# Kernel tuning notes

Hardware: AMD Instinct MI355X
Metric: run time of the kernel (lower is better)

## Reference

```python
import jax, jax.numpy as jnp
import numpy as np
from jax import lax

NUM_HEADS = 8
EPS = 1e-12  # torch F.normalize eps


def setup_inputs() -> dict:
    key = jax.random.key(0)
    ks = jax.random.split(key, 5)
    dim = 192
    b, h, w = 8, 128, 128
    return {
        "x": jax.random.normal(ks[0], (b, dim, h, w), jnp.float32),
        "w_qkv": jax.random.normal(ks[1], (3 * dim, dim, 1, 1), jnp.float32) * (1.0 / np.sqrt(dim)),
        "w_dw": jax.random.normal(ks[2], (3 * dim, 1, 3, 3), jnp.float32) * (1.0 / 3.0),
        "w_proj": jax.random.normal(ks[3], (dim, dim, 1, 1), jnp.float32) * (1.0 / np.sqrt(dim)),
        "temperature": jnp.ones((NUM_HEADS, 1, 1), jnp.float32),
    }


def _l2norm(t):
    n = jnp.sqrt(jnp.sum(t * t, axis=-1, keepdims=True))
    return t / jnp.maximum(n, EPS)


def reference(x, w_qkv, w_dw, w_proj, temperature):
    b, c, h, w = x.shape
    # 1x1 conv to 3*dim channels
    qkv = jnp.einsum('bchw,oc->bohw', x, w_qkv[:, :, 0, 0])
    # depthwise 3x3 conv, dilation=2, padding=2, groups=3*dim
    qkv = lax.conv_general_dilated(
        qkv, w_dw, window_strides=(1, 1), padding=((2, 2), (2, 2)),
        rhs_dilation=(2, 2), feature_group_count=3 * c,
        dimension_numbers=('NCHW', 'OIHW', 'NCHW'))
    q, k, v = jnp.split(qkv, 3, axis=1)
    ch = c // NUM_HEADS
    def heads(t):  # b (head ch) h w -> b head ch (h w)
        return t.reshape(b, NUM_HEADS, ch, h * w)
    q, k, v = heads(q), heads(k), heads(v)
    q = _l2norm(q)
    k = _l2norm(k)
    attn = jnp.einsum('bhcn,bhdn->bhcd', q, k) * temperature  # (b, head, ch, ch)
    attn = jax.nn.softmax(attn, axis=-1)
    out = jnp.einsum('bhcd,bhdn->bhcn', attn, v)
    out = out.reshape(b, c, h, w)
    out = jnp.einsum('bchw,oc->bohw', out, w_proj[:, :, 0, 0])
    return out
```

## Files before the change

### kernel.cpp

```cpp
#include <hip/hip_runtime.h>


#define DIM 192
#define NH 8
#define CH 24
#define IH 128
#define IW 128
#define NPIX (IH*IW)
#define BATCH 8
#define QKVC (3*DIM)
#define PAD 200
#define SPAD 264

typedef unsigned short u16;
typedef short bf16x8 __attribute__((ext_vector_type(8)));
typedef float f32x4 __attribute__((ext_vector_type(4)));

__device__ __forceinline__ float b2f(u16 u){
    unsigned v = ((unsigned)u) << 16;
    return __builtin_bit_cast(float, v);
}
__device__ __forceinline__ u16 f2b(float f){
    unsigned u = __builtin_bit_cast(unsigned, f);
    u += 0x7fffu + ((u >> 16) & 1u);
    return (u16)(u >> 16);
}

__device__ __forceinline__ void conv_row8(const u16* __restrict__ rp, int px0,
        float w0, float w1, float w2, float* o_){
    float f[12];
    if(px0 > 0){
        unsigned u = *(const unsigned*)(rp + px0 - 2);
        f[0] = b2f((u16)u); f[1] = b2f((u16)(u >> 16));
    } else { f[0] = 0.f; f[1] = 0.f; }
    bf16x8 v = *(const bf16x8*)(rp + px0);
    #pragma unroll
    for(int j=0;j<8;j++) f[2+j] = b2f((u16)v[j]);
    if(px0 < 120){
        unsigned u = *(const unsigned*)(rp + px0 + 8);
        f[10] = b2f((u16)u); f[11] = b2f((u16)(u >> 16));
    } else { f[10] = 0.f; f[11] = 0.f; }
    #pragma unroll
    for(int i=0;i<8;i++) o_[i] += w0*f[i] + w1*f[i+2] + w2*f[i+4];
}

__global__ __launch_bounds__(256) void k0_wcvt(const float* __restrict__ wqkv,
        u16* __restrict__ wb){
    int i = (blockIdx.x*256 + threadIdx.x)*4;
    f32x4 v = *(const f32x4*)&wqkv[i];
    unsigned lo = ((unsigned)f2b(v[1]) << 16) | f2b(v[0]);
    unsigned hi = ((unsigned)f2b(v[3]) << 16) | f2b(v[2]);
    *(uint2*)&wb[i] = make_uint2(lo, hi);
}

__global__ __launch_bounds__(256) void k1_qkv(const float* __restrict__ x,
        const u16* __restrict__ wb, u16* __restrict__ qkv_pre){
    __shared__ __align__(16) u16 Xl[128*PAD];
    const int tid = threadIdx.x;
    const int pt = blockIdx.x, b = blockIdx.y;
    const int p0 = pt*128;
    {
        const int px = tid & 127, half = tid >> 7;
        const float* xb = x + (size_t)b*DIM*NPIX + p0 + px;
        for(int cg = 0; cg < 12; cg++){
            int cb = half*96 + cg*8;
            bf16x8 v;
            #pragma unroll
            for(int j=0;j<8;j++) v[j] = (short)f2b(xb[(size_t)(cb+j)*NPIX]);
            *(bf16x8*)&Xl[px*PAD + cb] = v;
        }
    }
    __syncthreads();
    const int lane = tid & 63, w = tid >> 6;
    const int r = lane & 15, quad = lane >> 4;
    const int mbase = (w & 1)*32, nbase = (w >> 1)*64;
    u16* op = qkv_pre + (size_t)b*QKVC*NPIX + p0;
    for(int ot = 0; ot < 9; ot++){
        const int obase = ot*64;
        f32x4 acc[8];
        { f32x4 z = {0.f,0.f,0.f,0.f}; for(int i=0;i<8;i++) acc[i]=z; }
        const u16* w0p = wb + (size_t)(obase + mbase + r)*DIM;
        const u16* w1p = w0p + 16*DIM;
        #pragma unroll
        for(int kk = 0; kk < 6; kk++){
            const int k0 = kk*32 + quad*8;
            bf16x8 a0 = *(const bf16x8*)&w0p[k0];
            bf16x8 a1 = *(const bf16x8*)&w1p[k0];
            #pragma unroll
            for(int ni=0; ni<4; ni++){
                bf16x8 bb = *(const bf16x8*)&Xl[(nbase + ni*16 + r)*PAD + k0];
                acc[ni*2+0] = __builtin_amdgcn_mfma_f32_16x16x32_bf16(bb, a0, acc[ni*2+0], 0,0,0);
                acc[ni*2+1] = __builtin_amdgcn_mfma_f32_16x16x32_bf16(bb, a1, acc[ni*2+1], 0,0,0);
            }
        }
        #pragma unroll
        for(int ni=0; ni<4; ni++)
            #pragma unroll
            for(int mi=0; mi<2; mi++){
                int o = obase + mbase + mi*16 + r;
                int px = nbase + ni*16 + quad*4;
                f32x4 a = acc[ni*2+mi];
                unsigned lo = ((unsigned)f2b(a[1]) << 16) | f2b(a[0]);
                unsigned hi = ((unsigned)f2b(a[3]) << 16) | f2b(a[2]);
                *(uint2*)&op[(size_t)o*NPIX + px] = make_uint2(lo, hi);
            }
    }
}

__global__ __launch_bounds__(256) void k2_gram(const u16* __restrict__ qkv_pre,
        const float* __restrict__ wdw, float* __restrict__ G){
    __shared__ __align__(16) u16 Sl[48*SPAD];
    const int tid = threadIdx.x;
    const int pc = blockIdx.x, h = blockIdx.y, b = blockIdx.z;
    const int lane = tid & 63, w = tid >> 6;
    const int r = lane & 15, quad = lane >> 4;
    f32x4 acc[6];
    { f32x4 z = {0.f,0.f,0.f,0.f}; for(int i=0;i<6;i++) acc[i]=z; }
    for(int chunk = 0; chunk < 2; chunk++){
        if(chunk) __syncthreads();
        for(int it = 0; it < 6; it++){
            int t = tid + it*256;
            int c48 = t >> 5, oct = t & 31;
            int isK = (c48 >= CH);
            int c = isK ? (c48 - CH) : c48;
            int ch = (isK ? DIM : 0) + h*CH + c;
            const u16* base = qkv_pre + ((size_t)b*QKVC + ch)*NPIX;
            const float* wv = wdw + ch*9;
            int py = pc*4 + chunk*2 + (oct >> 4);
            int px0 = (oct & 15)*8;
            float o_[8];
            #pragma unroll
            for(int i=0;i<8;i++) o_[i]=0.f;
            #pragma unroll
            for(int ky=0;ky<3;ky++){
                int ry = py + 2*ky - 2;
                if(ry < 0 || ry >= IH) continue;
                conv_row8(base + ry*IW, px0, wv[ky*3], wv[ky*3+1], wv[ky*3+2], o_);
            }
            bf16x8 v;
            #pragma unroll
            for(int i=0;i<8;i++) v[i] = (short)f2b(o_[i]);
            *(bf16x8*)&Sl[c48*SPAD + oct*8] = v;
        }
        __syncthreads();
        #pragma unroll
        for(int kk = 0; kk < 2; kk++){
            const int k0 = w*64 + kk*32 + quad*8;
            bf16x8 f0 = *(const bf16x8*)&Sl[(     r)*SPAD + k0];
            bf16x8 f1 = *(const bf16x8*)&Sl[(16 + r)*SPAD + k0];
            bf16x8 f2 = *(const bf16x8*)&Sl[(32 + r)*SPAD + k0];
            acc[0] = __builtin_amdgcn_mfma_f32_16x16x32_bf16(f0, f0, acc[0], 0,0,0);
            acc[1] = __builtin_amdgcn_mfma_f32_16x16x32_bf16(f0, f1, acc[1], 0,0,0);
            acc[2] = __builtin_amdgcn_mfma_f32_16x16x32_bf16(f0, f2, acc[2], 0,0,0);
            acc[3] = __builtin_amdgcn_mfma_f32_16x16x32_bf16(f1, f1, acc[3], 0,0,0);
            acc[4] = __builtin_amdgcn_mfma_f32_16x16x32_bf16(f1, f2, acc[4], 0,0,0);
            acc[5] = __builtin_amdgcn_mfma_f32_16x16x32_bf16(f2, f2, acc[5], 0,0,0);
        }
    }
    __syncthreads();
    float* R = (float*)Sl;
    #pragma unroll
    for(int tile=0; tile<6; tile++)
        *(f32x4*)&R[(w*6 + tile)*256 + lane*4] = acc[tile];
    __syncthreads();
    float* Gb = G + (size_t)(b*NH + h)*48*48;
    #pragma unroll
    for(int i=0; i<6; i++){
        int idx = tid + i*256;
        int tile = idx >> 8, rem = idx & 255;
        int ln = rem >> 2, t = rem & 3;
        float s = R[idx] + R[1536 + idx] + R[2*1536 + idx] + R[3*1536 + idx];
        int ti = (tile<3) ? 0 : ((tile<5) ? 1 : 2);
        int tj = (tile<3) ? tile : ((tile<5) ? (tile-2) : 2);
        int c = ti*16 + (ln >> 4)*4 + t;
        int d = tj*16 + (ln & 15);
        atomicAdd(&Gb[c*48 + d], s);
    }
}

__global__ __launch_bounds__(256) void k4_vconv(u16* __restrict__ qkv_pre,
        const float* __restrict__ wdw){
    const int tid = threadIdx.x;
    const int oct = tid & 15, pyl = tid >> 4;
    const int band = blockIdx.x, cp = blockIdx.y, b = blockIdx.z;
    const int py = band*16 + pyl, px0 = oct*8;
    #pragma unroll
    for(int j=0;j<2;j++){
        int ch = cp*2 + j;
        const u16* base = qkv_pre + ((size_t)b*QKVC + 2*DIM + ch)*NPIX;
        const float* wv = wdw + (2*DIM + ch)*9;
        float o_[8];
        #pragma unroll
        for(int i=0;i<8;i++) o_[i]=0.f;
        #pragma unroll
        for(int ky=0;ky<3;ky++){
            int ry = py + 2*ky - 2;
            if(ry < 0 || ry >= IH) continue;
            conv_row8(base + ry*IW, px0, wv[ky*3], wv[ky*3+1], wv[ky*3+2], o_);
        }
        bf16x8 v;
        #pragma unroll
        for(int i=0;i<8;i++) v[i] = (short)f2b(o_[i]);
        *(bf16x8*)&qkv_pre[((size_t)b*QKVC + ch)*NPIX + py*IW + px0] = v;
    }
}

__global__ __launch_bounds__(256) void k3_attn(const float* __restrict__ G,
        const float* __restrict__ temp, const float* __restrict__ wproj,
        u16* __restrict__ M){
    __shared__ float attn[NH][CH][CH];
    __shared__ float nq[DIM], nk[DIM];
    const int b = blockIdx.x, tid = threadIdx.x;
    const float* Gb = G + (size_t)b*NH*48*48;
    if(tid < DIM){
        int h = tid / CH, c = tid % CH;
        const float* g = Gb + (size_t)h*48*48;
        nq[tid] = fmaxf(sqrtf(g[c*48 + c]), 1e-12f);
        nk[tid] = fmaxf(sqrtf(g[(CH+c)*48 + (CH+c)]), 1e-12f);
    }
    __syncthreads();
    if(tid < DIM){
        int h = tid / CH, c = tid % CH;
        float t = temp[h];
        const float* g = Gb + (size_t)h*48*48 + c*48 + CH;
        float row[CH];
        float mx = -1e30f;
        #pragma unroll
        for(int d=0; d<CH; d++){
            float v = g[d] / (nq[tid]*nk[h*CH+d]) * t;
            row[d]=v; mx = fmaxf(mx,v);
        }
        float sum=0.f;
        #pragma unroll
        for(int d=0;d<CH;d++){ row[d]=expf(row[d]-mx); sum+=row[d]; }
        float inv = 1.f/sum;
        #pragma unroll
        for(int d=0;d<CH;d++) attn[h][c][d] = row[d]*inv;
    }
    __syncthreads();
    u16* Mb = M + (size_t)b*DIM*DIM;
    for(int i = tid; i < DIM*DIM; i += 256){
        int o = i / DIM, hd = i % DIM;
        int h = hd / CH, d = hd % CH;
        float s = 0.f;
        #pragma unroll
        for(int c=0;c<CH;c++)
            s += wproj[o*DIM + h*CH + c] * attn[h][c][d];
        Mb[i] = f2b(s);
    }
}

__global__ __launch_bounds__(256) void k5_out(const u16* __restrict__ qkv_pre,
        const u16* __restrict__ M, float* __restrict__ out){
    __shared__ __align__(16) u16 vl[128*PAD];
    const int tid = threadIdx.x;
    const int py = blockIdx.x, b = blockIdx.y;
    const int p0 = py*IW;
    {
        const int px = tid & 127, half = tid >> 7;
        const u16* vb = qkv_pre + (size_t)b*QKVC*NPIX + p0 + px;
        for(int cg = 0; cg < 12; cg++){
            int cb = half*96 + cg*8;
            bf16x8 v;
            #pragma unroll
            for(int j=0;j<8;j++) v[j] = (short)vb[(size_t)(cb+j)*NPIX];
            *(bf16x8*)&vl[px*PAD + cb] = v;
        }
    }
    __syncthreads();
    const int lane = tid & 63, w = tid >> 6;
    const int r = lane & 15, quad = lane >> 4;
    const int mbase = (w & 1)*32, nbase = (w >> 1)*64;
    const u16* Mb = M + (size_t)b*DIM*DIM;
    for(int ot = 0; ot < 3; ot++){
        const int obase = ot*64;
        f32x4 acc[8];
        { f32x4 z = {0.f,0.f,0.f,0.f}; for(int i=0;i<8;i++) acc[i]=z; }
        const u16* m0 = Mb + (size_t)(obase + mbase + r)*DIM;
        const u16* m1 = m0 + 16*DIM;
        #pragma unroll
        for(int kk = 0; kk < 6; kk++){
            const int k0 = kk*32 + quad*8;
            bf16x8 a0 = *(const bf16x8*)&m0[k0];
            bf16x8 a1 = *(const bf16x8*)&m1[k0];
            #pragma unroll
            for(int ni=0; ni<4; ni++){
                bf16x8 bb = *(const bf16x8*)&vl[(nbase + ni*16 + r)*PAD + k0];
                acc[ni*2+0] = __builtin_amdgcn_mfma_f32_16x16x32_bf16(a0, bb, acc[ni*2+0], 0,0,0);
                acc[ni*2+1] = __builtin_amdgcn_mfma_f32_16x16x32_bf16(a1, bb, acc[ni*2+1], 0,0,0);
            }
        }
        float* op = out + ((size_t)b*DIM + obase)*NPIX + p0;
        #pragma unroll
        for(int ni=0; ni<4; ni++)
            #pragma unroll
            for(int mi=0; mi<2; mi++){
                int o_loc = mbase + mi*16 + quad*4;
                int p_loc = nbase + ni*16 + r;
                #pragma unroll
                for(int t=0;t<4;t++)
                    op[(size_t)(o_loc+t)*NPIX + p_loc] = acc[ni*2+mi][t];
            }
    }
}

extern "C" void kernel_launch(void* const* d_in, const int* in_sizes, int n_in,
                              void* d_out, int out_size, void* d_ws, size_t ws_size,
                              hipStream_t stream){
    const float* x     = (const float*)d_in[0];
    const float* wqkv  = (const float*)d_in[1];
    const float* wdw   = (const float*)d_in[2];
    const float* wproj = (const float*)d_in[3];
    const float* temp  = (const float*)d_in[4];
    float* out = (float*)d_out;

    char* ws = (char*)d_ws;
    u16* qkv_pre = (u16*)ws;
    size_t off = (size_t)BATCH*QKVC*NPIX*sizeof(u16);
    float* G  = (float*)(ws + off); off += (size_t)BATCH*NH*48*48*4;
    u16* M    = (u16*)(ws + off);   off += (size_t)BATCH*DIM*DIM*2;
    u16* wb   = (u16*)(ws + off);   off += (size_t)QKVC*DIM*2;

    hipMemsetAsync(G, 0, (size_t)BATCH*NH*48*48*sizeof(float), stream);

    k0_wcvt<<<108, 256, 0, stream>>>(wqkv, wb);
    k1_qkv <<<dim3(128, BATCH), 256, 0, stream>>>(x, wb, qkv_pre);
    k2_gram<<<dim3(32, NH, BATCH), 256, 0, stream>>>(qkv_pre, wdw, G);
    k4_vconv<<<dim3(8, 96, BATCH), 256, 0, stream>>>(qkv_pre, wdw);
    k3_attn<<<BATCH, 256, 0, stream>>>(G, temp, wproj, M);
    k5_out <<<dim3(128, BATCH), 256, 0, stream>>>(qkv_pre, M, out);
}
```

Baseline: 433.8 us.

## Halve pixel tiles in QKV and output GEMMs, split output channels per wave

Both the QKV projection and the output projection kernels now process 64 pixels per block instead of 128. That doubles the grid and halves LDS use per block, which should raise occupancy on the many-CU GPU. Each wave now owns a disjoint set of 16-row output-channel tiles across all 64 pixels, rather than a 32x64 quadrant. The output kernel swaps MFMA operand order so each lane writes contiguous pixels with a 16-byte vector store instead of scalar strided stores. In exchange, each weight fragment is reused across fewer pixels and each block re-reads the weights more often.

New measurement: 435.0 us. No clear change (+0.3%).

```diff
diff --git a/kernel.cpp b/kernel.cpp
--- a/kernel.cpp
+++ b/kernel.cpp
@@ -55,15 +55,16 @@
 
 __global__ __launch_bounds__(256) void k1_qkv(const float* __restrict__ x,
         const u16* __restrict__ wb, u16* __restrict__ qkv_pre){
-    __shared__ __align__(16) u16 Xl[128*PAD];
+    __shared__ __align__(16) u16 Xl[64*PAD];
     const int tid = threadIdx.x;
     const int pt = blockIdx.x, b = blockIdx.y;
-    const int p0 = pt*128;
+    const int p0 = pt*64;
     {
-        const int px = tid & 127, half = tid >> 7;
+        const int px = tid & 63, grp = tid >> 6;
         const float* xb = x + (size_t)b*DIM*NPIX + p0 + px;
-        for(int cg = 0; cg < 12; cg++){
-            int cb = half*96 + cg*8;
+        #pragma unroll
+        for(int cg = 0; cg < 6; cg++){
+            int cb = grp*48 + cg*8;
             bf16x8 v;
             #pragma unroll
             for(int j=0;j<8;j++) v[j] = (short)f2b(xb[(size_t)(cb+j)*NPIX]);
@@ -73,37 +74,31 @@
     __syncthreads();
     const int lane = tid & 63, w = tid >> 6;
     const int r = lane & 15, quad = lane >> 4;
-    const int mbase = (w & 1)*32, nbase = (w >> 1)*64;
     u16* op = qkv_pre + (size_t)b*QKVC*NPIX + p0;
-    for(int ot = 0; ot < 9; ot++){
-        const int obase = ot*64;
-        f32x4 acc[8];
-        { f32x4 z = {0.f,0.f,0.f,0.f}; for(int i=0;i<8;i++) acc[i]=z; }
-        const u16* w0p = wb + (size_t)(obase + mbase + r)*DIM;
-        const u16* w1p = w0p + 16*DIM;
+    for(int i = 0; i < 9; i++){
+        const int ob = (w*9 + i)*16;
+        f32x4 acc[4];
+        { f32x4 z = {0.f,0.f,0.f,0.f}; for(int j=0;j<4;j++) acc[j]=z; }
+        const u16* wp = wb + (size_t)(ob + r)*DIM;
         #pragma unroll
         for(int kk = 0; kk < 6; kk++){
             const int k0 = kk*32 + quad*8;
-            bf16x8 a0 = *(const bf16x8*)&w0p[k0];
-            bf16x8 a1 = *(const bf16x8*)&w1p[k0];
+            bf16x8 a0 = *(const bf16x8*)&wp[k0];
             #pragma unroll
             for(int ni=0; ni<4; ni++){
-                bf16x8 bb = *(const bf16x8*)&Xl[(nbase + ni*16 + r)*PAD + k0];
-                acc[ni*2+0] = __builtin_amdgcn_mfma_f32_16x16x32_bf16(bb, a0, acc[ni*2+0], 0,0,0);
-                acc[ni*2+1] = __builtin_amdgcn_mfma_f32_16x16x32_bf16(bb, a1, acc[ni*2+1], 0,0,0);
+                bf16x8 bb = *(const bf16x8*)&Xl[(ni*16 + r)*PAD + k0];
+                acc[ni] = __builtin_amdgcn_mfma_f32_16x16x32_bf16(bb, a0, acc[ni], 0,0,0);
             }
         }
         #pragma unroll
-        for(int ni=0; ni<4; ni++)
-            #pragma unroll
-            for(int mi=0; mi<2; mi++){
-                int o = obase + mbase + mi*16 + r;
-                int px = nbase + ni*16 + quad*4;
-                f32x4 a = acc[ni*2+mi];
-                unsigned lo = ((unsigned)f2b(a[1]) << 16) | f2b(a[0]);
-                unsigned hi = ((unsigned)f2b(a[3]) << 16) | f2b(a[2]);
-                *(uint2*)&op[(size_t)o*NPIX + px] = make_uint2(lo, hi);
-            }
+        for(int ni=0; ni<4; ni++){
+            int o = ob + r;
+            int px = ni*16 + quad*4;
+            f32x4 a = acc[ni];
+            unsigned lo = ((unsigned)f2b(a[1]) << 16) | f2b(a[0]);
+            unsigned hi = ((unsigned)f2b(a[3]) << 16) | f2b(a[2]);
+            *(uint2*)&op[(size_t)o*NPIX + px] = make_uint2(lo, hi);
+        }
     }
 }
 
@@ -252,15 +247,16 @@
 
 __global__ __launch_bounds__(256) void k5_out(const u16* __restrict__ qkv_pre,
         const u16* __restrict__ M, float* __restrict__ out){
-    __shared__ __align__(16) u16 vl[128*PAD];
+    __shared__ __align__(16) u16 vl[64*PAD];
     const int tid = threadIdx.x;
-    const int py = blockIdx.x, b = blockIdx.y;
-    const int p0 = py*IW;
+    const int pt = blockIdx.x, b = blockIdx.y;
+    const int p0 = pt*64;
     {
-        const int px = tid & 127, half = tid >> 7;
+        const int px = tid & 63, grp = tid >> 6;
         const u16* vb = qkv_pre + (size_t)b*QKVC*NPIX + p0 + px;
-        for(int cg = 0; cg < 12; cg++){
-            int cb = half*96 + cg*8;
+        #pragma unroll
+        for(int cg = 0; cg < 6; cg++){
+            int cb = grp*48 + cg*8;
             bf16x8 v;
             #pragma unroll
             for(int j=0;j<8;j++) v[j] = (short)vb[(size_t)(cb+j)*NPIX];
@@ -270,37 +266,26 @@
     __syncthreads();
     const int lane = tid & 63, w = tid >> 6;
     const int r = lane & 15, quad = lane >> 4;
-    const int mbase = (w & 1)*32, nbase = (w >> 1)*64;
     const u16* Mb = M + (size_t)b*DIM*DIM;
-    for(int ot = 0; ot < 3; ot++){
-        const int obase = ot*64;
-        f32x4 acc[8];
-        { f32x4 z = {0.f,0.f,0.f,0.f}; for(int i=0;i<8;i++) acc[i]=z; }
-        const u16* m0 = Mb + (size_t)(obase + mbase + r)*DIM;
-        const u16* m1 = m0 + 16*DIM;
+    float* op = out + (size_t)b*DIM*NPIX + p0;
+    for(int i = 0; i < 3; i++){
+        const int ob = (w*3 + i)*16;
+        f32x4 acc[4];
+        { f32x4 z = {0.f,0.f,0.f,0.f}; for(int j=0;j<4;j++) acc[j]=z; }
+        const u16* mp = Mb + (size_t)(ob + r)*DIM;
         #pragma unroll
         for(int kk = 0; kk < 6; kk++){
             const int k0 = kk*32 + quad*8;
-            bf16x8 a0 = *(const bf16x8*)&m0[k0];
-            bf16x8 a1 = *(const bf16x8*)&m1[k0];
+            bf16x8 a0 = *(const bf16x8*)&mp[k0];
             #pragma unroll
             for(int ni=0; ni<4; ni++){
-                bf16x8 bb = *(const bf16x8*)&vl[(nbase + ni*16 + r)*PAD + k0];
-                acc[ni*2+0] = __builtin_amdgcn_mfma_f32_16x16x32_bf16(a0, bb, acc[ni*2+0], 0,0,0);
-                acc[ni*2+1] = __builtin_amdgcn_mfma_f32_16x16x32_bf16(a1, bb, acc[ni*2+1], 0,0,0);
+                bf16x8 bb = *(const bf16x8*)&vl[(ni*16 + r)*PAD + k0];
+                acc[ni] = __builtin_amdgcn_mfma_f32_16x16x32_bf16(bb, a0, acc[ni], 0,0,0);
             }
         }
-        float* op = out + ((size_t)b*DIM + obase)*NPIX + p0;
         #pragma unroll
         for(int ni=0; ni<4; ni++)
-            #pragma unroll
-            for(int mi=0; mi<2; mi++){
-                int o_loc = mbase + mi*16 + quad*4;
-                int p_loc = nbase + ni*16 + r;
-                #pragma unroll
-                for(int t=0;t<4;t++)
-                    op[(size_t)(o_loc+t)*NPIX + p_loc] = acc[ni*2+mi][t];
-            }
+            *(f32x4*)&op[(size_t)(ob + r)*NPIX + ni*16 + quad*4] = acc[ni];
     }
 }
 
@@ -324,9 +309,9 @@
     hipMemsetAsync(G, 0, (size_t)BATCH*NH*48*48*sizeof(float), stream);
 
     k0_wcvt<<<108, 256, 0, stream>>>(wqkv, wb);
-    k1_qkv <<<dim3(128, BATCH), 256, 0, stream>>>(x, wb, qkv_pre);
+    k1_qkv <<<dim3(256, BATCH), 256, 0, stream>>>(x, wb, qkv_pre);
     k2_gram<<<dim3(32, NH, BATCH), 256, 0, stream>>>(qkv_pre, wdw, G);
     k4_vconv<<<dim3(8, 96, BATCH), 256, 0, stream>>>(qkv_pre, wdw);
     k3_attn<<<BATCH, 256, 0, stream>>>(G, temp, wproj, M);
-    k5_out <<<dim3(128, BATCH), 256, 0, stream>>>(qkv_pre, M, out);
-}
+    k5_out <<<dim3(256, BATCH), 256, 0, stream>>>(qkv_pre, M, out);
+}
```
